# Optimization experiments

Measured on AMD Instinct MI355X. Metric: run time of the kernel, lower is better.

Reference implementation:

```python
import jax, jax.numpy as jnp
import numpy as np

T, B, H, L = 2048, 32, 512, 2  # seq_len, batch, hidden(=input), num_layers
G = 4 * H
W_SCALE = 0.05  # keep randn-initialized weights out of deep gate saturation


def setup_inputs() -> dict:
    key = jax.random.key(0)
    ks = jax.random.split(key, 5)
    return {
        "x": jax.random.normal(ks[0], (T, B, H), dtype=jnp.float32),
        "w_ih": jax.random.normal(ks[1], (L, G, H), dtype=jnp.float32) * W_SCALE,
        "w_hh": jax.random.normal(ks[2], (L, G, H), dtype=jnp.float32) * W_SCALE,
        "b_ih": jax.random.normal(ks[3], (L, G), dtype=jnp.float32) * W_SCALE,
        "b_hh": jax.random.normal(ks[4], (L, G), dtype=jnp.float32) * W_SCALE,
        "h0": jnp.zeros((L, B, H), dtype=jnp.float32),
        "c0": jnp.zeros((L, B, H), dtype=jnp.float32),
    }


def _lstm_layer(x, w_ih, w_hh, b_ih, b_hh, h0, c0):
    # Precompute input-side gate contributions for all timesteps at once:
    # gates_x[t] = x[t] @ w_ih.T + b_ih + b_hh   (shape [T, B, 4H])
    gates_x = jnp.einsum("tbi,gi->tbg", x, w_ih) + b_ih + b_hh

    def step(carry, gx):
        h, c = carry
        gates = gx + h @ w_hh.T  # [B, 4H]
        i, f, g, o = jnp.split(gates, 4, axis=-1)  # chunk(4, 1) order: i,f,g,o
        i = jax.nn.sigmoid(i)
        f = jax.nn.sigmoid(f)
        g = jnp.tanh(g)
        o = jax.nn.sigmoid(o)
        c = f * c + i * g
        h = o * jnp.tanh(c)
        return (h, c), h

    (hT, cT), ys = jax.lax.scan(step, (h0, c0), gates_x)
    return ys, hT, cT


def reference(x, w_ih, w_hh, b_ih, b_hh, h0, c0):
    out = x
    h_fin, c_fin = [], []
    for l in range(L):  # small fixed stack of structurally identical layers
        out, hT, cT = _lstm_layer(out, w_ih[l], w_hh[l], b_ih[l], b_hh[l], h0[l], c0[l])
        h_fin.append(hT)
        c_fin.append(cT)
    return out, jnp.stack(h_fin), jnp.stack(c_fin)
```

## Files before the change

kernel.cpp:

```cpp
#include <hip/hip_runtime.h>
#include <hip/hip_bf16.h>
#include <stdint.h>

#define T_LEN 2048
#define BATCH 32
#define HID   512
#define GDIM  2048
#define NL    2
#define NBL   32
#define UPB   16
#define RSL   16
#define BH    (BATCH*HID)
#define SLOTB (BH*2)
#define RINGB (RSL*SLOTB)

#define FZ_FB   2048
#define FZ_DET  4096
#define FZ_ABT  4160
#define FZ_TOT  4224

typedef __attribute__((ext_vector_type(8))) __bf16         bf16x8;
typedef __attribute__((ext_vector_type(8))) unsigned short u16x8;
typedef __attribute__((ext_vector_type(4))) unsigned short u16x4;
typedef __attribute__((ext_vector_type(4))) float          f32x4;

__device__ __forceinline__ unsigned short f2bf(float f) {
  unsigned int u = __builtin_bit_cast(unsigned int, f);
  u += 0x7FFFu + ((u >> 16) & 1u);
  return (unsigned short)(u >> 16);
}
__device__ __forceinline__ f32x4 pack8(f32x4 a, f32x4 b) {
  u16x8 r;
  r[0]=f2bf(a[0]); r[1]=f2bf(a[1]); r[2]=f2bf(a[2]); r[3]=f2bf(a[3]);
  r[4]=f2bf(b[0]); r[5]=f2bf(b[1]); r[6]=f2bf(b[2]); r[7]=f2bf(b[3]);
  return __builtin_bit_cast(f32x4, r);
}
__device__ __forceinline__ float sigm(float x)  { return 1.0f / (1.0f + __expf(-x)); }
__device__ __forceinline__ float tanh_(float x) { return 2.0f / (1.0f + __expf(-2.0f*x)) - 1.0f; }

__device__ __forceinline__ f32x4 ld16_pl(const void* p)  { f32x4 r; asm volatile("global_load_dwordx4 %0, %1, off"     : "=v"(r) : "v"(p)); return r; }
__device__ __forceinline__ f32x4 ld16_sc0(const void* p) { f32x4 r; asm volatile("global_load_dwordx4 %0, %1, off sc0" : "=v"(r) : "v"(p)); return r; }
__device__ __forceinline__ f32x4 ld16_sc1(const void* p) { f32x4 r; asm volatile("global_load_dwordx4 %0, %1, off sc1" : "=v"(r) : "v"(p)); return r; }
__device__ __forceinline__ int lddww_sc1(const void* p) {
  int r; asm volatile("global_load_dword %0, %1, off sc1\n\ts_waitcnt vmcnt(0)" : "=v"(r) : "v"(p) : "memory"); return r;
}
__device__ __forceinline__ void st16_sc0(void* p, f32x4 v) { asm volatile("global_store_dwordx4 %0, %1, off sc0" :: "v"(p), "v"(v) : "memory"); }
__device__ __forceinline__ void st16_sc1(void* p, f32x4 v) { asm volatile("global_store_dwordx4 %0, %1, off sc1" :: "v"(p), "v"(v) : "memory"); }
__device__ __forceinline__ void stdw_sc1(void* p, int v) { asm volatile("global_store_dword %0, %1, off sc1" :: "v"(p), "v"(v) : "memory"); }
__device__ __forceinline__ void vm_drain() { asm volatile("s_waitcnt vmcnt(0)" ::: "memory"); }


__global__ void prep_misc(const float* __restrict__ b_ih, const float* __restrict__ b_hh,
                          const float* __restrict__ h0,
                          int* __restrict__ flagz, float* __restrict__ bsum,
                          char* __restrict__ ring0, char* __restrict__ ring1s) {
  int i = blockIdx.x * blockDim.x + threadIdx.x;
  if (i < FZ_TOT) flagz[i] = 0;
  if (i < NL*GDIM) bsum[i] = b_ih[i] + b_hh[i];
  if (i < NL*BH) {
    int layer = i >> 14, e = i & 16383;
    int b = e >> 9, u = e & 511;
    unsigned short v = f2bf(h0[((size_t)layer*BATCH + b)*HID + u]);
    size_t off = (size_t)(u >> 4)*1024 + (size_t)b*32 + (size_t)(u & 15)*2;
    *(unsigned short*)(ring0  + (size_t)layer*RINGB + off) = v;
    *(unsigned short*)(ring1s + (size_t)layer*RINGB + off) = v;
  }
}

__global__ void prep_w(const float* __restrict__ wih, const float* __restrict__ whh,
                       unsigned short* __restrict__ wihb, unsigned short* __restrict__ whhb) {
  const int n4 = NL*GDIM*HID/4;
  for (int i = blockIdx.x*blockDim.x + threadIdx.x; i < 2*n4; i += gridDim.x*blockDim.x) {
    const float*    src = (i < n4) ? wih  : whh;
    unsigned short* dst = (i < n4) ? wihb : whhb;
    int j = (i < n4) ? i : i - n4;
    f32x4 v = *((const f32x4*)src + j);
    u16x4 o; o[0]=f2bf(v[0]); o[1]=f2bf(v[1]); o[2]=f2bf(v[2]); o[3]=f2bf(v[3]);
    *((u16x4*)dst + j) = o;
  }
}


__global__ __launch_bounds__(512, 2) void lstm_persist(
    const float* __restrict__ x, const float* __restrict__ c0,
    const unsigned short* __restrict__ wihb, const unsigned short* __restrict__ whhb,
    const float* __restrict__ bsum,
    char* __restrict__ ring0, char* __restrict__ ring1s,
    int* __restrict__ flagz, float* __restrict__ out) {

  const int bid = blockIdx.x;
  const int r8  = bid & 7;
  if (r8 >= NL) return;
  const int layer = r8;
  const int lb    = bid >> 3;
  const int actIdx = layer*NBL + lb;
  const int tid  = threadIdx.x;
  const int lane = tid & 63;
  const int wave = tid >> 6;
  const int mh = wave & 1, nh = wave >> 1;
  const int col = lane & 15, kg = lane >> 4;
  const int gt  = col & 3;
  const int uu  = nh*4 + (col >> 2);
  const int u0  = lb * UPB;
  const int gu  = u0 + uu;
  const int grow = gt*HID + gu;
  const int tb  = mh*16 + kg*4 + gt;

  int* flagsA = flagz;
  int* flagsB = flagz + FZ_FB;
  int* detect = flagz + FZ_DET;
  int* abortp = flagz + FZ_ABT;

  __shared__ __align__(16) f32x4 smem[4096];
  __shared__ __align__(16) unsigned short hbuf16[512];
  __shared__ __align__(16) float houtf[512];

  f32x4 wfx[16], wfh[16];
  {
    const unsigned short* wxr = wihb + ((size_t)(layer*GDIM + grow))*HID + kg*8;
    const unsigned short* whr = whhb + ((size_t)(layer*GDIM + grow))*HID + kg*8;
#pragma unroll
    for (int ks = 0; ks < 16; ++ks) {
      wfx[ks] = *(const f32x4*)(wxr + ks*32);
      wfh[ks] = *(const f32x4*)(whr + ks*32);
    }
  }

  float c = c0[((size_t)layer*BATCH + tb)*HID + gu];
  const float bi  = bsum[layer*GDIM + 0*HID + gu];
  const float bfv = bsum[layer*GDIM + 1*HID + gu];
  const float bg  = bsum[layer*GDIM + 2*HID + gu];
  const float bo  = bsum[layer*GDIM + 3*HID + gu];

  char* ringF = ring0  + (size_t)layer*RINGB;
  char* ringS = ring1s + (size_t)layer*RINGB;
  const char* ringPrev = ring1s;
  int* myfA = flagsA + actIdx*32;
  int* myfB = flagsB + actIdx*32;
  const bool pl = lane < NBL;
  const int* fpOwnA = flagsA + (layer*NBL + lane)*32;
  const int* fpOthB = flagsB + ((1-layer)*NBL + lane)*32;
  int seenOwn = 0, seenOth = 0;
  bool dead = false;

  int xcc = 0;
  asm volatile("s_getreg_b32 %0, hwreg(HW_REG_XCC_ID)" : "=s"(xcc));
  if (tid == 0) stdw_sc1(detect + actIdx, xcc + 1);
  int dv = 0;
  {
    int spins = 0;
    for (;;) {
      if (dv == 0) dv = lddww_sc1(detect + lane);
      if (__all(dv != 0)) break;
      if (((++spins) & 255) == 0) {
        if (lddww_sc1(abortp)) { dead = true; break; }
        if (spins >= (1 << 20)) { stdw_sc1(abortp, 1); dead = true; break; }
      }
    }
  }
  const int dref0 = __shfl(dv, 0, 64), dref1 = __shfl(dv, 32, 64);
  const bool fastL0 = __all((lane < 32) ? (dv != 0 && dv == dref0) : 1);
  const bool fastL1 = __all((lane >= 32) ? (dv != 0 && dv == dref1) : 1);
  const bool fast = (layer ? fastL1 : fastL0) && !dead;

  int roff[4];
#pragma unroll
  for (int q = 0; q < 4; ++q) {
    int id = q*512 + tid;
    int mh2 = id >> 10, ks2 = (id >> 6) & 15, lf = id & 63;
    int ug = ks2*32 + (lf >> 4)*8;
    int batch = mh2*16 + (lf & 15);
    roff[q] = (ug >> 4)*1024 + batch*32 + (ug & 8)*2;
  }

  for (int t = 0; t < T_LEN; ++t) {
    const int slotR = t & (RSL-1);
    const int slotW = (t+1) & (RSL-1);

#pragma unroll
    for (int ks = 0; ks < 16; ++ks)
      asm volatile("" : "+v"(wfx[ks]), "+v"(wfh[ks]));

    f32x4 xpre[8];
    if (layer == 0) {
#pragma unroll
      for (int q = 0; q < 4; ++q) {
        int id = q*512 + tid;
        int mh2 = id >> 10, ks2 = (id >> 6) & 15, lf = id & 63;
        const float* s = x + ((size_t)t*BATCH + mh2*16 + (lf & 15))*HID + ks2*32 + (lf >> 4)*8;
        xpre[2*q]   = ld16_pl(s);
        xpre[2*q+1] = ld16_pl(s + 4);
      }
    }

    if (wave == 0 && !dead) {
      int spins = 0;
      while (!__all(pl ? (seenOwn >= t) : 1)) {
        if (pl && seenOwn < t) { int v = lddww_sc1(fpOwnA); if (v > seenOwn) seenOwn = v; }
        if (((++spins) & 255) == 0) {
          if (lddww_sc1(abortp)) { dead = true; break; }
          if (spins >= (1 << 21)) { stdw_sc1(abortp, 1); dead = true; break; }
        }
      }
    }
    if (wave == 1 && !dead) {
      const int tgt = (layer == 0) ? (t - 14) : (t + 1);
      int spins = 0;
      while (!__all(pl ? (seenOth >= tgt) : 1)) {
        if (pl && seenOth < tgt) { int v = lddww_sc1(fpOthB); if (v > seenOth) seenOth = v; }
        if (((++spins) & 255) == 0) {
          if (lddww_sc1(abortp)) { dead = true; break; }
          if (spins >= (1 << 21)) { stdw_sc1(abortp, 1); dead = true; break; }
        }
      }
    }
    __syncthreads();

    f32x4 xq[4], hq[4];
    if (layer == 1) {
      const char* p = ringPrev + (size_t)slotW*SLOTB;
#pragma unroll
      for (int q = 0; q < 4; ++q) xq[q] = ld16_sc1(p + roff[q]);
    }
    if (fast && t > 0) {
      const char* p = ringF + (size_t)slotR*SLOTB;
#pragma unroll
      for (int q = 0; q < 4; ++q) hq[q] = ld16_sc0(p + roff[q]);
    } else {
      const char* p = ringS + (size_t)slotR*SLOTB;
#pragma unroll
      for (int q = 0; q < 4; ++q) hq[q] = ld16_sc1(p + roff[q]);
    }
    vm_drain();

#pragma unroll
    for (int q = 0; q < 4; ++q) smem[q*512 + tid] = hq[q];
    if (layer == 0) {
#pragma unroll
      for (int q = 0; q < 4; ++q) smem[2048 + q*512 + tid] = pack8(xpre[2*q], xpre[2*q+1]);
    } else {
#pragma unroll
      for (int q = 0; q < 4; ++q) smem[2048 + q*512 + tid] = xq[q];
    }
    __syncthreads();

    if (layer == 1 && wave == 1 && lane == 0) stdw_sc1(myfB, t + 1);

    f32x4 accx = {0.f,0.f,0.f,0.f}, acch = {0.f,0.f,0.f,0.f};
    {
      const f32x4* hb = (const f32x4*)smem;
      const f32x4* xb = (const f32x4*)smem + 2048;
#pragma unroll
      for (int ks = 0; ks < 16; ++ks) {
        f32x4 ah = hb[(mh*16 + ks)*64 + lane];
        f32x4 av = xb[(mh*16 + ks)*64 + lane];
        accx = __builtin_amdgcn_mfma_f32_16x16x32_bf16(
                 __builtin_bit_cast(bf16x8, av), __builtin_bit_cast(bf16x8, wfx[ks]), accx, 0,0,0);
        acch = __builtin_amdgcn_mfma_f32_16x16x32_bf16(
                 __builtin_bit_cast(bf16x8, ah), __builtin_bit_cast(bf16x8, wfh[ks]), acch, 0,0,0);
      }
    }
    const f32x4 acc = accx + acch;

    float m0 = acc[0], m1 = acc[1], m2 = acc[2], m3 = acc[3];
    {
      float s0 = __shfl_xor(m0, 1), s1 = __shfl_xor(m1, 1),
            s2 = __shfl_xor(m2, 1), s3 = __shfl_xor(m3, 1);
      if (gt & 1) { m0 = s1; m2 = s3; } else { m1 = s0; m3 = s2; }
      s0 = __shfl_xor(m0, 2); s1 = __shfl_xor(m1, 2);
      s2 = __shfl_xor(m2, 2); s3 = __shfl_xor(m3, 2);
      if (gt & 2) { m0 = s2; m1 = s3; } else { m2 = s0; m3 = s1; }
    }
    const float iv = sigm(m0 + bi), fv = sigm(m1 + bfv);
    const float gv = tanh_(m2 + bg), ov = sigm(m3 + bo);
    c = fv*c + iv*gv;
    const float h = ov * tanh_(c);

    hbuf16[tb*16 + uu] = f2bf(h);
    if (layer == 1) houtf[tb*16 + uu] = h;
    if (t == T_LEN-1) {
      out[(size_t)T_LEN*BH + ((size_t)layer*BATCH + tb)*HID + gu] = h;
      out[(size_t)T_LEN*BH + (size_t)NL*BH + ((size_t)layer*BATCH + tb)*HID + gu] = c;
    }
    __syncthreads();

    if (wave == 0) {
      f32x4 v = *(const f32x4*)((const char*)hbuf16 + lane*16);
      char* d = (fast ? ringF : ringS) + (size_t)slotW*SLOTB + lb*1024 + lane*16;
      if (fast) st16_sc0(d, v); else st16_sc1(d, v);
      vm_drain();
      if (lane == 0) {
        stdw_sc1(myfA, t + 1);
        if (layer == 0 && !fast) stdw_sc1(myfB, t + 1);
      }
    } else if (wave == 1 && layer == 0 && fast) {
      f32x4 v = *(const f32x4*)((const char*)hbuf16 + lane*16);
      st16_sc1(ringS + (size_t)slotW*SLOTB + lb*1024 + lane*16, v);
      vm_drain();
      if (lane == 0) stdw_sc1(myfB, t + 1);
    } else if (layer == 1 && (wave == 2 || wave == 3)) {
      int l2 = (wave - 2)*64 + lane;
      int b2 = l2 >> 2, part = l2 & 3;
      f32x4 v = *(const f32x4*)((const char*)houtf + b2*64 + part*16);
      *(f32x4*)(out + (size_t)t*BH + (size_t)b2*HID + u0 + part*4) = v;
    }
  }

  vm_drain();
  __syncthreads();
  if (tid == 0) { stdw_sc1(myfA, T_LEN + 1); stdw_sc1(myfB, T_LEN + 1); }
}


extern "C" void kernel_launch(void* const* d_in, const int* in_sizes, int n_in,
                              void* d_out, int out_size, void* d_ws, size_t ws_size,
                              hipStream_t stream) {
  const float* x    = (const float*)d_in[0];
  const float* w_ih = (const float*)d_in[1];
  const float* w_hh = (const float*)d_in[2];
  const float* b_ih = (const float*)d_in[3];
  const float* b_hh = (const float*)d_in[4];
  const float* h0   = (const float*)d_in[5];
  const float* c0   = (const float*)d_in[6];
  float* out = (float*)d_out;

  char* ws = (char*)d_ws;
  size_t off = 0;
  auto alloc = [&](size_t bytes) -> void* {
    off = (off + 255) & ~(size_t)255;
    void* p = ws + off;
    off += bytes;
    return p;
  };
  int*            flagz = (int*)alloc((size_t)FZ_TOT * sizeof(int));
  float*          bsum  = (float*)alloc((size_t)NL*GDIM*sizeof(float));
  char*           ring0 = (char*)alloc((size_t)NL*RINGB);
  char*           ring1s= (char*)alloc((size_t)NL*RINGB);
  unsigned short* wihb  = (unsigned short*)alloc((size_t)NL*GDIM*HID*2);
  unsigned short* whhb  = (unsigned short*)alloc((size_t)NL*GDIM*HID*2);
  (void)ws_size;

  prep_misc<<<128, 256, 0, stream>>>(b_ih, b_hh, h0, flagz, bsum, ring0, ring1s);
  prep_w<<<1024, 256, 0, stream>>>(w_ih, w_hh, wihb, whhb);
  lstm_persist<<<256, 512, 0, stream>>>(x, c0, wihb, whhb, bsum,
                                        ring0, ring1s, flagz, out);
  (void)in_sizes; (void)n_in; (void)out_size;
}
```

Baseline: 8.745 ms.

## Pipeline flag polling with two in-flight loads and move publishing off polling waves

Replaces the serialized load-then-wait flag spin loops with a helper that keeps two flag loads in flight and checks them alternately, to shorten the latency of detecting a peer block's progress each timestep. All lanes now issue loads (masked to valid flag addresses) instead of only pending lanes. Ring publishing and flag stores move from waves 0/1 to waves 2/3 (or 4 for layer 1), so the polling waves do not also carry store drain latency into the next step's wait. The trade-off is more polling traffic to the flag lines and a change in which waves do the publishing work.

```diff
diff --git a/kernel.cpp b/kernel.cpp
--- a/kernel.cpp
+++ b/kernel.cpp
@@ -48,6 +48,33 @@
 __device__ __forceinline__ void st16_sc1(void* p, f32x4 v) { asm volatile("global_store_dwordx4 %0, %1, off sc1" :: "v"(p), "v"(v) : "memory"); }
 __device__ __forceinline__ void stdw_sc1(void* p, int v) { asm volatile("global_store_dword %0, %1, off sc1" :: "v"(p), "v"(v) : "memory"); }
 __device__ __forceinline__ void vm_drain() { asm volatile("s_waitcnt vmcnt(0)" ::: "memory"); }
+
+__device__ __forceinline__ void poll2sc1(const int* p, int tgt, int& seen,
+                                         bool pl, int* abortp, bool& dead) {
+  if (dead || __all(pl ? (seen >= tgt) : 1)) return;
+  int vA, vB;
+  asm volatile("global_load_dword %0, %1, off sc1" : "=v"(vA) : "v"(p));
+  asm volatile("global_load_dword %0, %1, off sc1" : "=v"(vB) : "v"(p));
+  int spins = 0;
+  for (;;) {
+    asm volatile("s_waitcnt vmcnt(1)" ::: "memory");
+    __builtin_amdgcn_sched_barrier(0);
+    if (pl && vA > seen) seen = vA;
+    if (__all(pl ? (seen >= tgt) : 1)) break;
+    asm volatile("global_load_dword %0, %1, off sc1" : "=v"(vA) : "v"(p));
+    asm volatile("s_waitcnt vmcnt(1)" ::: "memory");
+    __builtin_amdgcn_sched_barrier(0);
+    if (pl && vB > seen) seen = vB;
+    if (__all(pl ? (seen >= tgt) : 1)) break;
+    asm volatile("global_load_dword %0, %1, off sc1" : "=v"(vB) : "v"(p));
+    if (((spins += 2) & 255) <= 1) {
+      if (lddww_sc1(abortp)) { dead = true; break; }
+      if (spins >= (1 << 21)) { stdw_sc1(abortp, 1); dead = true; break; }
+    }
+  }
+  asm volatile("s_waitcnt vmcnt(0)" ::: "memory");
+  __builtin_amdgcn_sched_barrier(0);
+}
 
 
 __global__ void prep_misc(const float* __restrict__ b_ih, const float* __restrict__ b_hh,
@@ -138,8 +165,8 @@
   int* myfA = flagsA + actIdx*32;
   int* myfB = flagsB + actIdx*32;
   const bool pl = lane < NBL;
-  const int* fpOwnA = flagsA + (layer*NBL + lane)*32;
-  const int* fpOthB = flagsB + ((1-layer)*NBL + lane)*32;
+  const int* fpOwnA = flagsA + (layer*NBL + (lane & 31))*32;
+  const int* fpOthB = flagsB + ((1-layer)*NBL + (lane & 31))*32;
   int seenOwn = 0, seenOth = 0;
   bool dead = false;
 
@@ -173,6 +200,8 @@
     roff[q] = (ug >> 4)*1024 + batch*32 + (ug & 8)*2;
   }
 
+  const int pubw = (layer == 0) ? 2 : 4;
+
   for (int t = 0; t < T_LEN; ++t) {
     const int slotR = t & (RSL-1);
     const int slotW = (t+1) & (RSL-1);
@@ -193,27 +222,10 @@
       }
     }
 
-    if (wave == 0 && !dead) {
-      int spins = 0;
-      while (!__all(pl ? (seenOwn >= t) : 1)) {
-        if (pl && seenOwn < t) { int v = lddww_sc1(fpOwnA); if (v > seenOwn) seenOwn = v; }
-        if (((++spins) & 255) == 0) {
-          if (lddww_sc1(abortp)) { dead = true; break; }
-          if (spins >= (1 << 21)) { stdw_sc1(abortp, 1); dead = true; break; }
-        }
-      }
-    }
-    if (wave == 1 && !dead) {
-      const int tgt = (layer == 0) ? (t - 14) : (t + 1);
-      int spins = 0;
-      while (!__all(pl ? (seenOth >= tgt) : 1)) {
-        if (pl && seenOth < tgt) { int v = lddww_sc1(fpOthB); if (v > seenOth) seenOth = v; }
-        if (((++spins) & 255) == 0) {
-          if (lddww_sc1(abortp)) { dead = true; break; }
-          if (spins >= (1 << 21)) { stdw_sc1(abortp, 1); dead = true; break; }
-        }
-      }
-    }
+    if (wave == 0)
+      poll2sc1(fpOwnA, t, seenOwn, pl, abortp, dead);
+    if (wave == 1)
+      poll2sc1(fpOthB, (layer == 0) ? (t - 14) : (t + 1), seenOth, pl, abortp, dead);
     __syncthreads();
 
     f32x4 xq[4], hq[4];
@@ -284,7 +296,7 @@
     }
     __syncthreads();
 
-    if (wave == 0) {
+    if (wave == pubw) {
       f32x4 v = *(const f32x4*)((const char*)hbuf16 + lane*16);
       char* d = (fast ? ringF : ringS) + (size_t)slotW*SLOTB + lb*1024 + lane*16;
       if (fast) st16_sc0(d, v); else st16_sc1(d, v);
@@ -293,7 +305,7 @@
         stdw_sc1(myfA, t + 1);
         if (layer == 0 && !fast) stdw_sc1(myfB, t + 1);
       }
-    } else if (wave == 1 && layer == 0 && fast) {
+    } else if (wave == 3 && layer == 0 && fast) {
       f32x4 v = *(const f32x4*)((const char*)hbuf16 + lane*16);
       st16_sc1(ringS + (size_t)slotW*SLOTB + lb*1024 + lane*16, v);
       vm_drain();
```

New measurement: 9.131 ms. 4.4% more time.
